# Performance work log

Measured on AMD Instinct MI355X. Metric: run time of the kernel, lower is better.

Reference implementation:

```python
import jax, jax.numpy as jnp
from jax import lax
import numpy as np

D_MODEL, D_STATE, D_CONV, EXPAND = 1024, 16, 4, 2
D_INNER = EXPAND * D_MODEL          # 2048
DT_RANK = D_MODEL // 16             # 64
B_SZ, L_SEQ = 2, 2048


def setup_inputs() -> dict:
    key = jax.random.key(0)
    ks = jax.random.split(key, 8)
    x = jax.random.normal(ks[0], (B_SZ, L_SEQ, D_MODEL), jnp.float32)
    inp = {
        "x": x,
        "ln_g": jnp.ones((D_MODEL,), jnp.float32),
        "ln_b": jnp.zeros((D_MODEL,), jnp.float32),
        # fan-in scaled weights for numerical sanity
        "W_in": jax.random.normal(ks[1], (2 * D_INNER, D_MODEL), jnp.float32) / np.sqrt(D_MODEL),
        "conv_w": jax.random.normal(ks[2], (D_INNER, D_CONV), jnp.float32) / np.sqrt(D_CONV),
        "conv_b": jnp.zeros((D_INNER,), jnp.float32),
        "W_xp": jax.random.normal(ks[3], (DT_RANK + 2 * D_STATE, D_INNER), jnp.float32) / np.sqrt(D_INNER),
        "W_dt": jax.random.normal(ks[4], (D_INNER, DT_RANK), jnp.float32) / np.sqrt(DT_RANK),
        "b_dt": jax.random.normal(ks[5], (D_INNER,), jnp.float32) * 0.1 - 4.0,  # softplus(dt) small, like mamba init
        # S4D-real init: A = -exp(A_log), A_log = log(1..d_state)
        "A_log": jnp.broadcast_to(jnp.log(jnp.arange(1, D_STATE + 1, dtype=jnp.float32)), (D_INNER, D_STATE)).copy(),
        "D": jnp.ones((D_INNER,), jnp.float32),
        "W_out": jax.random.normal(ks[6], (D_MODEL, D_INNER), jnp.float32) / np.sqrt(D_INNER),
    }
    return inp


def _selective_scan(u, dt, A, Bm, Cm, Dvec):
    # u, dt: (B, L, d_inner); Bm, Cm: (B, L, d_state); A: (d_inner, d_state)
    def step(h, inputs):
        u_t, dt_t, B_t, C_t = inputs                      # (B,di),(B,di),(B,n),(B,n)
        dA = jnp.exp(dt_t[:, :, None] * A[None])          # (B,di,n), in (0,1) since A<0
        dBu = (dt_t * u_t)[:, :, None] * B_t[:, None, :]  # (B,di,n)
        h = dA * h + dBu
        y = jnp.einsum('bdn,bn->bd', h, C_t)
        return h, y
    xs = (u.transpose(1, 0, 2), dt.transpose(1, 0, 2),
          Bm.transpose(1, 0, 2), Cm.transpose(1, 0, 2))
    h0 = jnp.zeros((u.shape[0], u.shape[2], A.shape[1]), u.dtype)
    _, ys = lax.scan(step, h0, xs)
    return ys.transpose(1, 0, 2) + u * Dvec               # (B, L, d_inner)


def reference(x, ln_g, ln_b, W_in, conv_w, conv_b, W_xp, W_dt, b_dt, A_log, D, W_out):
    d_inner, d_conv = conv_w.shape
    dt_rank = W_dt.shape[1]
    d_state = A_log.shape[1]
    # pre-LayerNorm
    mu = jnp.mean(x, axis=-1, keepdims=True)
    var = jnp.mean(jnp.square(x - mu), axis=-1, keepdims=True)
    xn = (x - mu) * lax.rsqrt(var + 1e-5) * ln_g + ln_b
    # input projection -> (B, L, 2*d_inner)
    xz = jnp.einsum('bld,ed->ble', xn, W_in)
    u, z = jnp.split(xz, 2, axis=-1)
    # causal depthwise conv over time
    u_c = lax.conv_general_dilated(
        u.transpose(0, 2, 1),                 # (B, d_inner, L)
        conv_w[:, None, :],                   # (d_inner, 1, d_conv)
        window_strides=(1,), padding=[(d_conv - 1, 0)],
        feature_group_count=d_inner)
    u_c = jax.nn.silu((u_c + conv_b[None, :, None]).transpose(0, 2, 1))  # (B, L, d_inner)
    # data-dependent dt, B, C
    x_dbl = jnp.einsum('bld,ed->ble', u_c, W_xp)
    dt, Bm, Cm = jnp.split(x_dbl, [dt_rank, dt_rank + d_state], axis=-1)
    dt = jax.nn.softplus(jnp.einsum('blr,dr->bld', dt, W_dt) + b_dt)
    A = -jnp.exp(A_log)
    y = _selective_scan(u_c, dt, A, Bm, Cm, D)
    y = y * jax.nn.silu(z)
    out = jnp.einsum('ble,de->bld', y, W_out)
    return x + out
```

## Files before the change

### kernel.cpp

```cpp
#include <hip/hip_runtime.h>

typedef __bf16 bf16x8 __attribute__((ext_vector_type(8)));
typedef float  f32x4  __attribute__((ext_vector_type(4)));

#define LOG2E 1.44269504088896f

__device__ __forceinline__ float bfl(unsigned short s) {
    return __uint_as_float(((unsigned int)s) << 16);
}
__device__ __forceinline__ unsigned short f2bf(float f) {
    unsigned int x = __float_as_uint(f);
    x += 0x7fffu + ((x >> 16) & 1u);
    return (unsigned short)(x >> 16);
}
__device__ __forceinline__ float fexp2(float x) { return __builtin_amdgcn_exp2f(x); }
__device__ __forceinline__ float fexp(float x)  { return __builtin_amdgcn_exp2f(x * LOG2E); }
__device__ __forceinline__ float frcp(float x)  { return __builtin_amdgcn_rcpf(x); }
__device__ __forceinline__ float silu_f(float x) {
    return x * frcp(1.f + fexp2(-x * LOG2E));
}
__device__ __forceinline__ void gl_lds(const unsigned short* g, unsigned short* l) {
    __builtin_amdgcn_global_load_lds(
        (__attribute__((address_space(1))) const void*)g,
        (__attribute__((address_space(3))) void*)l, 16, 0, 0);
}

#define BSZ   2
#define LSEQ  2048
#define DMODEL 1024
#define DI    2048
#define DS    16
#define NCH   64
#define CL    32

#define WI_N   4194304
#define WXP_N  196608
#define WDT_N  131072
#define WOUT_N 2097152
#define WSEG1  (WI_N)
#define WSEG2  (WI_N + WXP_N)
#define WSEG3  (WI_N + WXP_N + WDT_N)
#define WTOT   (WI_N + WXP_N + WDT_N + WOUT_N)

__global__ __launch_bounds__(256) void cvt_weights(
    const float* __restrict__ w0, const float* __restrict__ w1,
    const float* __restrict__ w2, const float* __restrict__ w3,
    unsigned short* __restrict__ dst)
{
    const size_t e0 = ((size_t)blockIdx.x * 256 + threadIdx.x) * 8;
    if (e0 >= WTOT) return;
    const float* src;
    size_t off;
    if      (e0 < WSEG1) { src = w0; off = e0; }
    else if (e0 < WSEG2) { src = w1; off = e0 - WSEG1; }
    else if (e0 < WSEG3) { src = w2; off = e0 - WSEG2; }
    else                 { src = w3; off = e0 - WSEG3; }
    float4 a = *(const float4*)(src + off);
    float4 b = *(const float4*)(src + off + 4);
    ushort4 lo, hi;
    lo.x = f2bf(a.x); lo.y = f2bf(a.y); lo.z = f2bf(a.z); lo.w = f2bf(a.w);
    hi.x = f2bf(b.x); hi.y = f2bf(b.y); hi.z = f2bf(b.z); hi.w = f2bf(b.w);
    *(ushort4*)(dst + e0) = lo;
    *(ushort4*)(dst + e0 + 4) = hi;
}

__global__ __launch_bounds__(256) void ln_kernel(
    const float* __restrict__ x,
    const float* __restrict__ g,
    const float* __restrict__ b,
    unsigned short* __restrict__ xn)
{
    const int row = blockIdx.x;
    const int tid = threadIdx.x;
    const int lane = tid & 63, wv = tid >> 6;
    const float* xp = x + (size_t)row * DMODEL;

    float4 v = ((const float4*)xp)[tid];
    float s = v.x + v.y + v.z + v.w;
    float q = v.x*v.x + v.y*v.y + v.z*v.z + v.w*v.w;
    #pragma unroll
    for (int o = 32; o > 0; o >>= 1) {
        s += __shfl_down(s, o);
        q += __shfl_down(q, o);
    }
    __shared__ float ss[4], sq[4];
    if (lane == 0) { ss[wv] = s; sq[wv] = q; }
    __syncthreads();
    s = ss[0] + ss[1] + ss[2] + ss[3];
    q = sq[0] + sq[1] + sq[2] + sq[3];
    const float mu  = s * (1.f / DMODEL);
    const float var = q * (1.f / DMODEL) - mu * mu;
    const float rs  = rsqrtf(var + 1e-5f);

    float4 gv = ((const float4*)g)[tid];
    float4 bv = ((const float4*)b)[tid];
    ushort4 o;
    o.x = f2bf((v.x - mu) * rs * gv.x + bv.x);
    o.y = f2bf((v.y - mu) * rs * gv.y + bv.y);
    o.z = f2bf((v.z - mu) * rs * gv.z + bv.z);
    o.w = f2bf((v.w - mu) * rs * gv.w + bv.w);
    ((ushort4*)(xn + (size_t)row * DMODEL))[tid] = o;
}

template<int EPI, int LOGM>
__global__ __launch_bounds__(512, 2) void gemm_pipe256(
    const unsigned short* __restrict__ A,
    const unsigned short* __restrict__ Bw,
    void* __restrict__ Cout,
    const void* __restrict__ aux0,
    int K, int ldc)
{
    __shared__ unsigned short As[2][256 * 64];
    __shared__ unsigned short Bs[2][256 * 64];
    const int tid  = threadIdx.x;
    const int lane = tid & 63;
    const int wid  = tid >> 6;
    const int wm   = (wid >> 2) * 128;
    const int wn   = (wid & 3) * 64;

    const int nwg = gridDim.x;
    const int id  = blockIdx.x;
    const int swz = (id & 7) * (nwg >> 3) + (id >> 3);
    const int bx  = swz & ((1 << LOGM) - 1);
    const int by  = swz >> LOGM;
    const size_t am0 = (size_t)bx * 256;
    const size_t bn0 = (size_t)by * 256;

    const int srow  = lane >> 3;
    const int sslot = (lane & 7) ^ srow;
    const unsigned short* gA = A  + (am0 + wid * 8 + srow) * (size_t)K + sslot * 8;
    const unsigned short* gB = Bw + (bn0 + wid * 8 + srow) * (size_t)K + sslot * 8;

    const int NT = K >> 6;

#define STAGE256(buf, ko)                                                      \
    {   _Pragma("unroll")                                                      \
        for (int j = 0; j < 4; ++j)                                            \
            gl_lds(gA + (size_t)(j * 64) * K + (ko), &As[buf][(j * 64 + wid * 8) * 64]); \
        _Pragma("unroll")                                                      \
        for (int j = 0; j < 4; ++j)                                            \
            gl_lds(gB + (size_t)(j * 64) * K + (ko), &Bs[buf][(j * 64 + wid * 8) * 64]); }

    STAGE256(0, 0)
    STAGE256(1, 64)

    f32x4 acc[8][4];
    f32x4 z4 = {0.f, 0.f, 0.f, 0.f};
    #pragma unroll
    for (int i = 0; i < 8; ++i)
        #pragma unroll
        for (int j = 0; j < 4; ++j) acc[i][j] = z4;

    const int lr  = lane & 15;
    const int lq  = lane >> 4;
    const int key = lr & 7;

#define RD_A(dst, q)                                                           \
    _Pragma("unroll")                                                          \
    for (int i = 0; i < 2; ++i)                                                \
        _Pragma("unroll")                                                      \
        for (int ks = 0; ks < 2; ++ks)                                         \
            dst[i][ks] = *(const bf16x8*)&As[cur][(wm + ((q) * 2 + i) * 16 + lr) * 64 \
                                                  + (((ks * 4 + lq) ^ key) * 8)];

#define MFMA_Q(src, q)                                                         \
    _Pragma("unroll")                                                          \
    for (int i = 0; i < 2; ++i)                                                \
        _Pragma("unroll")                                                      \
        for (int fn = 0; fn < 4; ++fn) {                                       \
            acc[(q) * 2 + i][fn] = __builtin_amdgcn_mfma_f32_16x16x32_bf16(    \
                src[i][0], bfv[fn][0], acc[(q) * 2 + i][fn], 0, 0, 0);         \
            acc[(q) * 2 + i][fn] = __builtin_amdgcn_mfma_f32_16x16x32_bf16(    \
                src[i][1], bfv[fn][1], acc[(q) * 2 + i][fn], 0, 0, 0);         }

    for (int t = 0; t < NT; ++t) {
        const int cur = t & 1;
        if (t < NT - 1) asm volatile("s_waitcnt vmcnt(8)" ::: "memory");
        else            asm volatile("s_waitcnt vmcnt(0)" ::: "memory");
        __builtin_amdgcn_s_barrier();
        __builtin_amdgcn_sched_barrier(0);

        bf16x8 bfv[4][2], fA[2][2], fB[2][2];
        #pragma unroll
        for (int fn = 0; fn < 4; ++fn)
            #pragma unroll
            for (int ks = 0; ks < 2; ++ks)
                bfv[fn][ks] = *(const bf16x8*)&Bs[cur][(wn + fn * 16 + lr) * 64
                                                        + (((ks * 4 + lq) ^ key) * 8)];
        RD_A(fA, 0)
        asm volatile("s_waitcnt lgkmcnt(0)" ::: "memory");
        __builtin_amdgcn_sched_barrier(0);

        RD_A(fB, 1)
        __builtin_amdgcn_s_setprio(1);
        MFMA_Q(fA, 0)
        __builtin_amdgcn_s_setprio(0);
        asm volatile("s_waitcnt lgkmcnt(0)" ::: "memory");
        __builtin_amdgcn_sched_barrier(0);

        RD_A(fA, 2)
        __builtin_amdgcn_s_setprio(1);
        MFMA_Q(fB, 1)
        __builtin_amdgcn_s_setprio(0);
        asm volatile("s_waitcnt lgkmcnt(0)" ::: "memory");
        __builtin_amdgcn_sched_barrier(0);

        RD_A(fB, 3)
        __builtin_amdgcn_s_setprio(1);
        MFMA_Q(fA, 2)
        __builtin_amdgcn_s_setprio(0);
        asm volatile("s_waitcnt lgkmcnt(0)" ::: "memory");
        __builtin_amdgcn_sched_barrier(0);

        __builtin_amdgcn_s_barrier();
        if (t + 2 < NT) {
            STAGE256(cur, (size_t)(t + 2) * 64)
        }
        __builtin_amdgcn_s_setprio(1);
        MFMA_Q(fB, 3)
        __builtin_amdgcn_s_setprio(0);
    }
#undef RD_A
#undef MFMA_Q
#undef STAGE256

    asm volatile("s_waitcnt vmcnt(0) lgkmcnt(0)" ::: "memory");
    __builtin_amdgcn_s_barrier();

    const int er = lq * 4;
    const int ec = lr;
    if constexpr (EPI == 0) {
        unsigned short* cw = &As[0][0] + wid * (16 * 88);
        const int rl  = lane >> 2;
        const int c8l = lane & 3;
        unsigned short* cbase = (unsigned short*)Cout;
        #pragma unroll
        for (int fm = 0; fm < 8; ++fm) {
            #pragma unroll
            for (int fn = 0; fn < 4; ++fn)
                #pragma unroll
                for (int r = 0; r < 4; ++r)
                    cw[(er + r) * 88 + fn * 16 + ec] = f2bf(acc[fm][fn][r]);
            #pragma unroll
            for (int u = 0; u < 2; ++u) {
                const int c8 = c8l + 4 * u;
                bf16x8 v = *(const bf16x8*)&cw[rl * 88 + c8 * 8];
                const size_t row = am0 + wm + fm * 16 + rl;
                const size_t col = bn0 + wn + c8 * 8;
                *(bf16x8*)(cbase + row * (size_t)ldc + col) = v;
            }
        }
    } else {
        #pragma unroll
        for (int fm = 0; fm < 8; ++fm) {
            #pragma unroll
            for (int fn = 0; fn < 4; ++fn) {
                const size_t col = bn0 + wn + fn * 16 + ec;
                #pragma unroll
                for (int r = 0; r < 4; ++r) {
                    const size_t row = am0 + wm + fm * 16 + er + r;
                    float t2 = acc[fm][fn][r] + ((const float*)aux0)[row * ldc + col];
                    ((float*)Cout)[row * ldc + col] = t2;
                }
            }
        }
    }
}

template<int EPI, int LOGNB>
__global__ __launch_bounds__(512, 2) void gemm_pipe128(
    const unsigned short* __restrict__ A,
    const unsigned short* __restrict__ Bw,
    void* __restrict__ Cout,
    const void* __restrict__ aux0,
    int K, int ldc)
{
    __shared__ unsigned short As[2][128 * 64];
    __shared__ unsigned short Bs[2][128 * 64];
    const int tid  = threadIdx.x;
    const int lane = tid & 63;
    const int wid  = tid >> 6;
    const int wm   = (wid >> 2) * 64;
    const int wn   = (wid & 3) * 32;

    const int nwg = gridDim.x;
    const int id  = blockIdx.x;
    const int swz = (id & 7) * (nwg >> 3) + (id >> 3);
    const int bn_i = swz & ((1 << LOGNB) - 1);
    const int bm_i = swz >> LOGNB;
    const size_t am0 = (size_t)bm_i * 128;
    const size_t bn0 = (size_t)bn_i * 128;

    const int srow  = lane >> 3;
    const int sslot = (lane & 7) ^ srow;
    const unsigned short* gA = A  + (am0 + wid * 16 + srow) * (size_t)K + sslot * 8;
    const unsigned short* gB = Bw + (bn0 + wid * 16 + srow) * (size_t)K + sslot * 8;

    const int NT = K >> 6;

#define STAGE128(buf, ko)                                                      \
    {   _Pragma("unroll")                                                      \
        for (int j = 0; j < 2; ++j)                                            \
            gl_lds(gA + (size_t)(j * 8) * K + (ko), &As[buf][(wid * 16 + j * 8) * 64]); \
        _Pragma("unroll")                                                      \
        for (int j = 0; j < 2; ++j)                                            \
            gl_lds(gB + (size_t)(j * 8) * K + (ko), &Bs[buf][(wid * 16 + j * 8) * 64]); }

    STAGE128(0, 0)
    STAGE128(1, 64)

    f32x4 acc[4][2];
    f32x4 z4 = {0.f, 0.f, 0.f, 0.f};
    #pragma unroll
    for (int i = 0; i < 4; ++i) { acc[i][0] = z4; acc[i][1] = z4; }

    const int lr  = lane & 15;
    const int lq  = lane >> 4;
    const int key = lr & 7;

#define RD_A128(dst, h)                                                        \
    _Pragma("unroll")                                                          \
    for (int i = 0; i < 2; ++i)                                                \
        _Pragma("unroll")                                                      \
        for (int ks = 0; ks < 2; ++ks)                                         \
            dst[i][ks] = *(const bf16x8*)&As[cur][(wm + ((h) * 2 + i) * 16 + lr) * 64 \
                                                  + (((ks * 4 + lq) ^ key) * 8)];

#define MFMA_H(src, h)                                                         \
    _Pragma("unroll")                                                          \
    for (int i = 0; i < 2; ++i)                                                \
        _Pragma("unroll")                                                      \
        for (int fn = 0; fn < 2; ++fn) {                                       \
            acc[(h) * 2 + i][fn] = __builtin_amdgcn_mfma_f32_16x16x32_bf16(    \
                src[i][0], bfv[fn][0], acc[(h) * 2 + i][fn], 0, 0, 0);         \
            acc[(h) * 2 + i][fn] = __builtin_amdgcn_mfma_f32_16x16x32_bf16(    \
                src[i][1], bfv[fn][1], acc[(h) * 2 + i][fn], 0, 0, 0);         }

    for (int t = 0; t < NT; ++t) {
        const int cur = t & 1;
        if (t < NT - 1) asm volatile("s_waitcnt vmcnt(4)" ::: "memory");
        else            asm volatile("s_waitcnt vmcnt(0)" ::: "memory");
        __builtin_amdgcn_s_barrier();
        __builtin_amdgcn_sched_barrier(0);

        bf16x8 bfv[2][2], fA[2][2], fB[2][2];
        #pragma unroll
        for (int fn = 0; fn < 2; ++fn)
            #pragma unroll
            for (int ks = 0; ks < 2; ++ks)
                bfv[fn][ks] = *(const bf16x8*)&Bs[cur][(wn + fn * 16 + lr) * 64
                                                        + (((ks * 4 + lq) ^ key) * 8)];
        RD_A128(fA, 0)
        asm volatile("s_waitcnt lgkmcnt(0)" ::: "memory");
        __builtin_amdgcn_sched_barrier(0);

        RD_A128(fB, 1)
        __builtin_amdgcn_s_setprio(1);
        MFMA_H(fA, 0)
        __builtin_amdgcn_s_setprio(0);
        asm volatile("s_waitcnt lgkmcnt(0)" ::: "memory");
        __builtin_amdgcn_sched_barrier(0);

        __builtin_amdgcn_s_barrier();
        if (t + 2 < NT) {
            STAGE128(cur, (size_t)(t + 2) * 64)
        }
        __builtin_amdgcn_s_setprio(1);
        MFMA_H(fB, 1)
        __builtin_amdgcn_s_setprio(0);
    }
#undef RD_A128
#undef MFMA_H
#undef STAGE128

    const int er = lq * 4;
    const int ec = lr;
    #pragma unroll
    for (int fm = 0; fm < 4; ++fm) {
        #pragma unroll
        for (int fn = 0; fn < 2; ++fn) {
            const size_t col = bn0 + wn + fn * 16 + ec;
            #pragma unroll
            for (int r = 0; r < 4; ++r) {
                const size_t row = am0 + wm + fm * 16 + er + r;
                float v = acc[fm][fn][r];
                if constexpr (EPI == 0) {
                    ((unsigned short*)Cout)[row * ldc + col] = f2bf(v);
                } else {
                    float t2 = v + ((const float*)aux0)[row * ldc + col];
                    ((float*)Cout)[row * ldc + col] = t2;
                }
            }
        }
    }
}

template<int BM, int BN, int EPI, int LOG_NBXM>
__global__ __launch_bounds__(256) void gemm_lds(
    const unsigned short* __restrict__ A,
    const unsigned short* __restrict__ Bw,
    void* __restrict__ Cout,
    const void* __restrict__ aux0,
    int K, int ldc)
{
    constexpr int FM = BM / 32;
    constexpr int FN = BN / 32;
    __shared__ unsigned short As[BM * 64];
    __shared__ unsigned short Bs[BN * 64];
    const int tid  = threadIdx.x;
    const int lane = tid & 63;
    const int wv   = tid >> 6;
    const int wm   = (wv >> 1) * (BM / 2);
    const int wn   = (wv & 1)  * (BN / 2);

    const int nwg = gridDim.x;
    const int id  = blockIdx.x;
    const int swz = (id & 7) * (nwg >> 3) + (id >> 3);
    const int bx  = swz & ((1 << LOG_NBXM) - 1);
    const int by  = swz >> LOG_NBXM;

    f32x4 acc[FM][FN];
    f32x4 z4 = {0.f, 0.f, 0.f, 0.f};
    #pragma unroll
    for (int i = 0; i < FM; ++i)
        #pragma unroll
        for (int j = 0; j < FN; ++j) acc[i][j] = z4;

    const size_t am0 = (size_t)bx * BM;
    const size_t bn0 = (size_t)by * BN;
    const int srow  = lane >> 3;
    const int scol  = (lane & 7) * 8;

    for (int k0 = 0; k0 < K; k0 += 64) {
        __syncthreads();
        #pragma unroll
        for (int i = 0; i < BM / 32; ++i) {
            const int rb = (wv * (BM / 32) + i) * 8;
            gl_lds(&A[(am0 + rb + srow) * (size_t)K + k0 + scol], &As[rb * 64]);
        }
        #pragma unroll
        for (int i = 0; i < BN / 32; ++i) {
            const int rb = (wv * (BN / 32) + i) * 8;
            gl_lds(&Bw[(bn0 + rb + srow) * (size_t)K + k0 + scol], &Bs[rb * 64]);
        }
        __syncthreads();
        const int lr = lane & 15, lk = (lane >> 4) * 8;
        #pragma unroll
        for (int ks = 0; ks < 2; ++ks) {
            bf16x8 af[FM], bfv[FN];
            #pragma unroll
            for (int fm = 0; fm < FM; ++fm)
                af[fm] = *(const bf16x8*)&As[(wm + fm * 16 + lr) * 64 + ks * 32 + lk];
            #pragma unroll
            for (int fn = 0; fn < FN; ++fn)
                bfv[fn] = *(const bf16x8*)&Bs[(wn + fn * 16 + lr) * 64 + ks * 32 + lk];
            #pragma unroll
            for (int fm = 0; fm < FM; ++fm)
                #pragma unroll
                for (int fn = 0; fn < FN; ++fn)
                    acc[fm][fn] = __builtin_amdgcn_mfma_f32_16x16x32_bf16(
                        af[fm], bfv[fn], acc[fm][fn], 0, 0, 0);
        }
    }

    const int er = (lane >> 4) * 4;
    const int ec = lane & 15;
    #pragma unroll
    for (int fm = 0; fm < FM; ++fm) {
        #pragma unroll
        for (int fn = 0; fn < FN; ++fn) {
            const size_t col = bn0 + wn + fn * 16 + ec;
            #pragma unroll
            for (int r = 0; r < 4; ++r) {
                const size_t row = am0 + wm + fm * 16 + er + r;
                float v = acc[fm][fn][r];
                if constexpr (EPI == 0) {
                    ((unsigned short*)Cout)[row * ldc + col] = f2bf(v);
                } else if constexpr (EPI == 2) {
                    float t = v + ((const float*)aux0)[col];
                    float e = fexp2(t * LOG2E);
                    float sp = 0.69314718056f * __builtin_amdgcn_logf(1.f + e);
                    if (t > 20.f) sp = t;
                    ((unsigned short*)Cout)[row * ldc + col] = f2bf(sp);
                } else {
                    float t = v + ((const float*)aux0)[row * ldc + col];
                    ((float*)Cout)[row * ldc + col] = t;
                }
            }
        }
    }
}

__global__ __launch_bounds__(256) void gemm4_splitk(
    const unsigned short* __restrict__ A,
    const unsigned short* __restrict__ Bw,
    float* __restrict__ Cpart)
{
    constexpr int LDP = 72;
    __shared__ unsigned short As[64 * LDP];
    __shared__ unsigned short Bs[96 * LDP];
    const int tid  = threadIdx.x;
    const int lane = tid & 63;
    const int wv   = tid >> 6;
    const int wm   = (wv >> 1) * 32;
    const int wn   = (wv & 1)  * 48;

    f32x4 acc[2][3];
    f32x4 z4 = {0.f, 0.f, 0.f, 0.f};
    #pragma unroll
    for (int i = 0; i < 2; ++i)
        #pragma unroll
        for (int j = 0; j < 3; ++j) acc[i][j] = z4;

    const size_t am0 = (size_t)blockIdx.x * 64;
    const int kz = blockIdx.y;
    const int kbeg = kz * 256;
    const int r0 = tid >> 3;
    const int c0 = (tid & 7) * 8;

    for (int k0 = kbeg; k0 < kbeg + 256; k0 += 64) {
        __syncthreads();
        #pragma unroll
        for (int p = 0; p < 2; ++p) {
            int r = r0 + p * 32;
            *(uint4*)&As[r * LDP + c0] = *(const uint4*)&A[(am0 + r) * (size_t)2048 + k0 + c0];
        }
        #pragma unroll
        for (int p = 0; p < 3; ++p) {
            int r = r0 + p * 32;
            *(uint4*)&Bs[r * LDP + c0] = *(const uint4*)&Bw[(size_t)r * 2048 + k0 + c0];
        }
        __syncthreads();
        const int lr = lane & 15, lk = (lane >> 4) * 8;
        #pragma unroll
        for (int ks = 0; ks < 2; ++ks) {
            bf16x8 af[2], bfv[3];
            #pragma unroll
            for (int fm = 0; fm < 2; ++fm)
                af[fm] = *(const bf16x8*)&As[(wm + fm * 16 + lr) * LDP + ks * 32 + lk];
            #pragma unroll
            for (int fn = 0; fn < 3; ++fn)
                bfv[fn] = *(const bf16x8*)&Bs[(wn + fn * 16 + lr) * LDP + ks * 32 + lk];
            #pragma unroll
            for (int fm = 0; fm < 2; ++fm)
                #pragma unroll
                for (int fn = 0; fn < 3; ++fn)
                    acc[fm][fn] = __builtin_amdgcn_mfma_f32_16x16x32_bf16(
                        af[fm], bfv[fn], acc[fm][fn], 0, 0, 0);
        }
    }

    const int er = (lane >> 4) * 4;
    const int ec = lane & 15;
    float* out = Cpart + (size_t)kz * 4096 * 96;
    #pragma unroll
    for (int fm = 0; fm < 2; ++fm) {
        #pragma unroll
        for (int fn = 0; fn < 3; ++fn) {
            const int col = wn + fn * 16 + ec;
            #pragma unroll
            for (int r = 0; r < 4; ++r) {
                const size_t row = am0 + wm + fm * 16 + er + r;
                out[row * 96 + col] = acc[fm][fn][r];
            }
        }
    }
}

__global__ __launch_bounds__(256) void reduce_xdbl(
    const float* __restrict__ Cpart,
    float* __restrict__ x_dbl,
    unsigned short* __restrict__ dtlow)
{
    const int e = blockIdx.x * 256 + threadIdx.x;
    float s = 0.f;
    #pragma unroll
    for (int kz = 0; kz < 8; ++kz) s += Cpart[(size_t)kz * 393216 + e];
    x_dbl[e] = s;
    const int row = e / 96, col = e - row * 96;
    if (col < 64) dtlow[row * 64 + col] = f2bf(s);
}

__global__ __launch_bounds__(256) void conv_silu(
    const unsigned short* __restrict__ xz,
    const float* __restrict__ convw,
    const float* __restrict__ convb,
    unsigned short* __restrict__ u_c)
{
    const size_t i = (size_t)blockIdx.x * 256 + threadIdx.x;
    if (i >= (size_t)BSZ * LSEQ * DI) return;
    const int d = (int)(i & (DI - 1));
    const size_t bl = i >> 11;
    const int l = (int)(bl & (LSEQ - 1));
    const int b = (int)(bl >> 11);

    float4 wv = *(const float4*)&convw[d * 4];
    float acc = convb[d];
    const size_t rowbase = (size_t)(b * LSEQ) * (2 * DI) + d;
    if (l >= 3) acc += bfl(xz[rowbase + (size_t)(l - 3) * (2 * DI)]) * wv.x;
    if (l >= 2) acc += bfl(xz[rowbase + (size_t)(l - 2) * (2 * DI)]) * wv.y;
    if (l >= 1) acc += bfl(xz[rowbase + (size_t)(l - 1) * (2 * DI)]) * wv.z;
    acc += bfl(xz[rowbase + (size_t)l * (2 * DI)]) * wv.w;
    u_c[i] = f2bf(silu_f(acc));
}

__device__ __forceinline__ bool load_A(const float* __restrict__ A_log, int d, float* An2) {
    bool fast = true;
    #pragma unroll
    for (int i = 0; i < 4; ++i) {
        float4 a = *(const float4*)&A_log[(size_t)d * DS + i * 4];
        float e0 = fexp(a.x), e1 = fexp(a.y), e2 = fexp(a.z), e3 = fexp(a.w);
        fast = fast && fabsf(e0 - (4*i+1)) < 1e-3f * (4*i+1)
                    && fabsf(e1 - (4*i+2)) < 1e-3f * (4*i+2)
                    && fabsf(e2 - (4*i+3)) < 1e-3f * (4*i+3)
                    && fabsf(e3 - (4*i+4)) < 1e-3f * (4*i+4);
        An2[4*i+0] = -e0 * LOG2E; An2[4*i+1] = -e1 * LOG2E;
        An2[4*i+2] = -e2 * LOG2E; An2[4*i+3] = -e3 * LOG2E;
    }
    return fast;
}

__global__ __launch_bounds__(256) void scan1(
    const unsigned short* __restrict__ dt,
    const unsigned short* __restrict__ u_c,
    const float* __restrict__ x_dbl,
    const float* __restrict__ A_log,
    float* __restrict__ chunk_h,
    float* __restrict__ Ssum)
{
    const int d = blockIdx.x * 256 + threadIdx.x;
    const int b = blockIdx.y, c = blockIdx.z;
    const int tid = threadIdx.x;

    __shared__ float sB[CL][DS];
    if (tid < 128) {
        int s = tid >> 2, j = (tid & 3) * 4;
        *(float4*)&sB[s][j] =
            *(const float4*)&x_dbl[(size_t)(b * LSEQ + c * CL + s) * 96 + 64 + j];
    }

    float An2[DS];
    const bool fast = load_A(A_log, d, An2);
    __syncthreads();

    float h[DS];
    #pragma unroll
    for (int n = 0; n < DS; ++n) h[n] = 0.f;
    float S = 0.f;
    const size_t base = (size_t)(b * LSEQ + c * CL) * DI + d;
    if (fast) {
        for (int s = 0; s < CL; ++s) {
            float dtt = bfl(dt[base + (size_t)s * DI]);
            float ut  = bfl(u_c[base + (size_t)s * DI]);
            S += dtt;
            float dtu = dtt * ut;
            float e1 = fexp2(-dtt * LOG2E);
            float p = 1.f;
            #pragma unroll
            for (int n = 0; n < DS; ++n) {
                p *= e1;
                h[n] = p * h[n] + dtu * sB[s][n];
            }
        }
    } else {
        for (int s = 0; s < CL; ++s) {
            float dtt = bfl(dt[base + (size_t)s * DI]);
            float ut  = bfl(u_c[base + (size_t)s * DI]);
            S += dtt;
            float dtu = dtt * ut;
            #pragma unroll
            for (int n = 0; n < DS; ++n) {
                float dA = fexp2(dtt * An2[n]);
                h[n] = dA * h[n] + dtu * sB[s][n];
            }
        }
    }
    const size_t co = ((size_t)((b * NCH + c) * DI) + d) * DS;
    #pragma unroll
    for (int n = 0; n < DS; ++n) chunk_h[co + n] = h[n];
    Ssum[(size_t)(b * NCH + c) * DI + d] = S;
}

__global__ __launch_bounds__(256) void scan2(
    float* __restrict__ chunk_h,
    const float* __restrict__ Ssum,
    const float* __restrict__ A_log)
{
    const int gid = blockIdx.x * 256 + threadIdx.x;
    const int b = gid >> 15;
    const int rem = gid & 32767;
    const int d = rem >> 4;
    const int n = rem & 15;
    const float A2 = -fexp(A_log[(size_t)d * DS + n]) * LOG2E;
    float H = 0.f;
    for (int c = 0; c < NCH; ++c) {
        const size_t idx = ((size_t)((b * NCH + c) * DI) + d) * DS + n;
        float hl = chunk_h[idx];
        float S  = Ssum[(size_t)(b * NCH + c) * DI + d];
        chunk_h[idx] = H;
        H = fexp2(A2 * S) * H + hl;
    }
}

__global__ __launch_bounds__(256) void scan3(
    const unsigned short* __restrict__ dt,
    const unsigned short* __restrict__ u_c,
    const float* __restrict__ x_dbl,
    const float* __restrict__ A_log,
    const float* __restrict__ Hstart,
    const float* __restrict__ Dvec,
    const unsigned short* __restrict__ xz,
    unsigned short* __restrict__ yb)
{
    const int d = blockIdx.x * 256 + threadIdx.x;
    const int b = blockIdx.y, c = blockIdx.z;
    const int tid = threadIdx.x;

    __shared__ float sBC[CL][32];
    {
        int s = tid >> 3, j = (tid & 7) * 4;
        *(float4*)&sBC[s][j] =
            *(const float4*)&x_dbl[(size_t)(b * LSEQ + c * CL + s) * 96 + 64 + j];
    }

    float An2[DS];
    const bool fast = load_A(A_log, d, An2);
    const float Dd = Dvec[d];
    float h[DS];
    const size_t co = ((size_t)((b * NCH + c) * DI) + d) * DS;
    #pragma unroll
    for (int n = 0; n < DS; ++n) h[n] = Hstart[co + n];
    __syncthreads();

    const size_t base  = (size_t)(b * LSEQ + c * CL) * DI + d;
    const size_t zbase = (size_t)(b * LSEQ + c * CL) * (2 * DI) + DI + d;
    if (fast) {
        for (int s = 0; s < CL; ++s) {
            float dtt = bfl(dt[base + (size_t)s * DI]);
            float ut  = bfl(u_c[base + (size_t)s * DI]);
            float dtu = dtt * ut;
            float e1 = fexp2(-dtt * LOG2E);
            float p = 1.f;
            float a0 = 0.f, a1 = 0.f;
            #pragma unroll
            for (int n = 0; n < DS; ++n) {
                p *= e1;
                h[n] = p * h[n] + dtu * sBC[s][n];
                if (n & 1) a1 += h[n] * sBC[s][16 + n];
                else       a0 += h[n] * sBC[s][16 + n];
            }
            float y = a0 + a1 + Dd * ut;
            float z = bfl(xz[zbase + (size_t)s * (2 * DI)]);
            yb[base + (size_t)s * DI] = f2bf(y * silu_f(z));
        }
    } else {
        for (int s = 0; s < CL; ++s) {
            float dtt = bfl(dt[base + (size_t)s * DI]);
            float ut  = bfl(u_c[base + (size_t)s * DI]);
            float dtu = dtt * ut;
            float a0 = 0.f, a1 = 0.f;
            #pragma unroll
            for (int n = 0; n < DS; ++n) {
                float dA = fexp2(dtt * An2[n]);
                h[n] = dA * h[n] + dtu * sBC[s][n];
                if (n & 1) a1 += h[n] * sBC[s][16 + n];
                else       a0 += h[n] * sBC[s][16 + n];
            }
            float y = a0 + a1 + Dd * ut;
            float z = bfl(xz[zbase + (size_t)s * (2 * DI)]);
            yb[base + (size_t)s * DI] = f2bf(y * silu_f(z));
        }
    }
}

extern "C" void kernel_launch(void* const* d_in, const int* in_sizes, int n_in,
                              void* d_out, int out_size, void* d_ws, size_t ws_size,
                              hipStream_t stream) {
    const float* x      = (const float*)d_in[0];
    const float* ln_g   = (const float*)d_in[1];
    const float* ln_b   = (const float*)d_in[2];
    const float* W_in   = (const float*)d_in[3];
    const float* conv_w = (const float*)d_in[4];
    const float* conv_b = (const float*)d_in[5];
    const float* W_xp   = (const float*)d_in[6];
    const float* W_dt   = (const float*)d_in[7];
    const float* b_dt   = (const float*)d_in[8];
    const float* A_log  = (const float*)d_in[9];
    const float* Dv     = (const float*)d_in[10];
    const float* W_out  = (const float*)d_in[11];
    float* out = (float*)d_out;

    char* w = (char*)d_ws;
    unsigned short* xn     = (unsigned short*)(w + 0);
    unsigned short* xz     = (unsigned short*)(w + 8388608);
    unsigned short* u_c    = (unsigned short*)(w + 41943040);
    float*          x_dbl  = (float*)         (w + 58720256);
    unsigned short* dtlow  = (unsigned short*)(w + 60293120);
    unsigned short* dtb    = (unsigned short*)(w + 60817408);
    float*          chunkh = (float*)         (w + 77594624);
    float*          Ssum   = (float*)         (w + 94371840);
    unsigned short* yb     = (unsigned short*)(w + 95420416);
    unsigned short* wbf    = (unsigned short*)(w + 112197632);
    float*          Cpart  = (float*)         (w + 125435904);
    unsigned short* Wi_bf   = wbf;
    unsigned short* Wxp_bf  = wbf + WSEG1;
    unsigned short* Wdt_bf  = wbf + WSEG2;
    unsigned short* Wout_bf = wbf + WSEG3;
    (void)in_sizes; (void)n_in; (void)out_size; (void)ws_size;

    const int MROWS = BSZ * LSEQ;

    cvt_weights<<<(WTOT / 8 + 255) / 256, 256, 0, stream>>>(
        W_in, W_xp, W_dt, W_out, wbf);
    ln_kernel<<<MROWS, 256, 0, stream>>>(x, ln_g, ln_b, xn);
    gemm_pipe256<0, 4><<<256, 512, 0, stream>>>(
        xn, Wi_bf, xz, nullptr, DMODEL, 2 * DI);
    conv_silu<<<(MROWS * DI) / 256, 256, 0, stream>>>(xz, conv_w, conv_b, u_c);
    gemm4_splitk<<<dim3(64, 8), 256, 0, stream>>>(u_c, Wxp_bf, Cpart);
    reduce_xdbl<<<(MROWS * 96) / 256, 256, 0, stream>>>(Cpart, x_dbl, dtlow);
    gemm_lds<128, 64, 2, 5><<<1024, 256, 0, stream>>>(
        dtlow, Wdt_bf, dtb, b_dt, 64, DI);
    scan1<<<dim3(DI / 256, BSZ, NCH), 256, 0, stream>>>(
        dtb, u_c, x_dbl, A_log, chunkh, Ssum);
    scan2<<<(BSZ * DI * DS) / 256, 256, 0, stream>>>(chunkh, Ssum, A_log);
    scan3<<<dim3(DI / 256, BSZ, NCH), 256, 0, stream>>>(
        dtb, u_c, x_dbl, A_log, chunkh, Dv, xz, yb);
    gemm_pipe128<3, 3><<<256, 512, 0, stream>>>(
        yb, Wout_bf, out, x, DI, DMODEL);
}
```

Measured before the change: 180.0 us.

## Merge layernorm with weight conversion, fold z-silu into GEMM epilogue, lengthen scan chunks

Merges the weight-conversion and layernorm kernels into one launch by splitting blocks between the two jobs. Applies silu to the z half of the input projection inside the GEMM epilogue, so the scan's final pass only multiplies by the stored value. Doubles the scan chunk length (32 to 64) and halves the chunk count, adjusting the shared-memory B/C loads to match. Fewer chunks mean less chunk-carry work but less parallelism in scan1 and scan3, and the z tensor is now stored after silu in bf16.

After: 188.5 us. +4.7%, slower.

```diff
diff --git a/kernel.cpp b/kernel.cpp
--- a/kernel.cpp
+++ b/kernel.cpp
@@ -30,8 +30,8 @@
 #define DMODEL 1024
 #define DI    2048
 #define DS    16
-#define NCH   64
-#define CL    32
+#define NCH   32
+#define CL    64
 
 #define WI_N   4194304
 #define WXP_N  196608
@@ -41,65 +41,65 @@
 #define WSEG2  (WI_N + WXP_N)
 #define WSEG3  (WI_N + WXP_N + WDT_N)
 #define WTOT   (WI_N + WXP_N + WDT_N + WOUT_N)
-
-__global__ __launch_bounds__(256) void cvt_weights(
+#define CVT_BLOCKS 3232
+
+__global__ __launch_bounds__(256) void ln_cvt(
+    const float* __restrict__ x,
+    const float* __restrict__ g,
+    const float* __restrict__ b,
+    unsigned short* __restrict__ xn,
     const float* __restrict__ w0, const float* __restrict__ w1,
     const float* __restrict__ w2, const float* __restrict__ w3,
     unsigned short* __restrict__ dst)
 {
-    const size_t e0 = ((size_t)blockIdx.x * 256 + threadIdx.x) * 8;
-    if (e0 >= WTOT) return;
-    const float* src;
-    size_t off;
-    if      (e0 < WSEG1) { src = w0; off = e0; }
-    else if (e0 < WSEG2) { src = w1; off = e0 - WSEG1; }
-    else if (e0 < WSEG3) { src = w2; off = e0 - WSEG2; }
-    else                 { src = w3; off = e0 - WSEG3; }
-    float4 a = *(const float4*)(src + off);
-    float4 b = *(const float4*)(src + off + 4);
-    ushort4 lo, hi;
-    lo.x = f2bf(a.x); lo.y = f2bf(a.y); lo.z = f2bf(a.z); lo.w = f2bf(a.w);
-    hi.x = f2bf(b.x); hi.y = f2bf(b.y); hi.z = f2bf(b.z); hi.w = f2bf(b.w);
-    *(ushort4*)(dst + e0) = lo;
-    *(ushort4*)(dst + e0 + 4) = hi;
-}
-
-__global__ __launch_bounds__(256) void ln_kernel(
-    const float* __restrict__ x,
-    const float* __restrict__ g,
-    const float* __restrict__ b,
-    unsigned short* __restrict__ xn)
-{
-    const int row = blockIdx.x;
     const int tid = threadIdx.x;
-    const int lane = tid & 63, wv = tid >> 6;
-    const float* xp = x + (size_t)row * DMODEL;
-
-    float4 v = ((const float4*)xp)[tid];
-    float s = v.x + v.y + v.z + v.w;
-    float q = v.x*v.x + v.y*v.y + v.z*v.z + v.w*v.w;
-    #pragma unroll
-    for (int o = 32; o > 0; o >>= 1) {
-        s += __shfl_down(s, o);
-        q += __shfl_down(q, o);
-    }
-    __shared__ float ss[4], sq[4];
-    if (lane == 0) { ss[wv] = s; sq[wv] = q; }
-    __syncthreads();
-    s = ss[0] + ss[1] + ss[2] + ss[3];
-    q = sq[0] + sq[1] + sq[2] + sq[3];
-    const float mu  = s * (1.f / DMODEL);
-    const float var = q * (1.f / DMODEL) - mu * mu;
-    const float rs  = rsqrtf(var + 1e-5f);
-
-    float4 gv = ((const float4*)g)[tid];
-    float4 bv = ((const float4*)b)[tid];
-    ushort4 o;
-    o.x = f2bf((v.x - mu) * rs * gv.x + bv.x);
-    o.y = f2bf((v.y - mu) * rs * gv.y + bv.y);
-    o.z = f2bf((v.z - mu) * rs * gv.z + bv.z);
-    o.w = f2bf((v.w - mu) * rs * gv.w + bv.w);
-    ((ushort4*)(xn + (size_t)row * DMODEL))[tid] = o;
+    if (blockIdx.x < BSZ * LSEQ) {
+        const int row = blockIdx.x;
+        const int lane = tid & 63, wv = tid >> 6;
+        const float* xp = x + (size_t)row * DMODEL;
+
+        float4 v = ((const float4*)xp)[tid];
+        float s = v.x + v.y + v.z + v.w;
+        float q = v.x*v.x + v.y*v.y + v.z*v.z + v.w*v.w;
+        #pragma unroll
+        for (int o = 32; o > 0; o >>= 1) {
+            s += __shfl_down(s, o);
+            q += __shfl_down(q, o);
+        }
+        __shared__ float ss[4], sq[4];
+        if (lane == 0) { ss[wv] = s; sq[wv] = q; }
+        __syncthreads();
+        s = ss[0] + ss[1] + ss[2] + ss[3];
+        q = sq[0] + sq[1] + sq[2] + sq[3];
+        const float mu  = s * (1.f / DMODEL);
+        const float var = q * (1.f / DMODEL) - mu * mu;
+        const float rs  = rsqrtf(var + 1e-5f);
+
+        float4 gv = ((const float4*)g)[tid];
+        float4 bv = ((const float4*)b)[tid];
+        ushort4 o;
+        o.x = f2bf((v.x - mu) * rs * gv.x + bv.x);
+        o.y = f2bf((v.y - mu) * rs * gv.y + bv.y);
+        o.z = f2bf((v.z - mu) * rs * gv.z + bv.z);
+        o.w = f2bf((v.w - mu) * rs * gv.w + bv.w);
+        ((ushort4*)(xn + (size_t)row * DMODEL))[tid] = o;
+    } else {
+        const size_t e0 = ((size_t)(blockIdx.x - BSZ * LSEQ) * 256 + tid) * 8;
+        if (e0 >= WTOT) return;
+        const float* src;
+        size_t off;
+        if      (e0 < WSEG1) { src = w0; off = e0; }
+        else if (e0 < WSEG2) { src = w1; off = e0 - WSEG1; }
+        else if (e0 < WSEG3) { src = w2; off = e0 - WSEG2; }
+        else                 { src = w3; off = e0 - WSEG3; }
+        float4 a = *(const float4*)(src + off);
+        float4 bb = *(const float4*)(src + off + 4);
+        ushort4 lo, hi;
+        lo.x = f2bf(a.x);  lo.y = f2bf(a.y);  lo.z = f2bf(a.z);  lo.w = f2bf(a.w);
+        hi.x = f2bf(bb.x); hi.y = f2bf(bb.y); hi.z = f2bf(bb.z); hi.w = f2bf(bb.w);
+        *(ushort4*)(dst + e0) = lo;
+        *(ushort4*)(dst + e0 + 4) = hi;
+    }
 }
 
 template<int EPI, int LOGM>
@@ -230,6 +230,7 @@
     const int er = lq * 4;
     const int ec = lr;
     if constexpr (EPI == 0) {
+        const bool zhalf = (bn0 >= (size_t)DI);
         unsigned short* cw = &As[0][0] + wid * (16 * 88);
         const int rl  = lane >> 2;
         const int c8l = lane & 3;
@@ -239,8 +240,11 @@
             #pragma unroll
             for (int fn = 0; fn < 4; ++fn)
                 #pragma unroll
-                for (int r = 0; r < 4; ++r)
-                    cw[(er + r) * 88 + fn * 16 + ec] = f2bf(acc[fm][fn][r]);
+                for (int r = 0; r < 4; ++r) {
+                    float v = acc[fm][fn][r];
+                    if (zhalf) v = silu_f(v);
+                    cw[(er + r) * 88 + fn * 16 + ec] = f2bf(v);
+                }
             #pragma unroll
             for (int u = 0; u < 2; ++u) {
                 const int c8 = c8l + 4 * u;
@@ -633,7 +637,7 @@
     const int tid = threadIdx.x;
 
     __shared__ float sB[CL][DS];
-    if (tid < 128) {
+    {
         int s = tid >> 2, j = (tid & 3) * 4;
         *(float4*)&sB[s][j] =
             *(const float4*)&x_dbl[(size_t)(b * LSEQ + c * CL + s) * 96 + 64 + j];
@@ -718,9 +722,11 @@
 
     __shared__ float sBC[CL][32];
     {
-        int s = tid >> 3, j = (tid & 7) * 4;
+        int s = tid >> 2, j = (tid & 3) * 8;
         *(float4*)&sBC[s][j] =
             *(const float4*)&x_dbl[(size_t)(b * LSEQ + c * CL + s) * 96 + 64 + j];
+        *(float4*)&sBC[s][j + 4] =
+            *(const float4*)&x_dbl[(size_t)(b * LSEQ + c * CL + s) * 96 + 64 + j + 4];
     }
 
     float An2[DS];
@@ -750,8 +756,8 @@
                 else       a0 += h[n] * sBC[s][16 + n];
             }
             float y = a0 + a1 + Dd * ut;
-            float z = bfl(xz[zbase + (size_t)s * (2 * DI)]);
-            yb[base + (size_t)s * DI] = f2bf(y * silu_f(z));
+            float zs = bfl(xz[zbase + (size_t)s * (2 * DI)]);
+            yb[base + (size_t)s * DI] = f2bf(y * zs);
         }
     } else {
         for (int s = 0; s < CL; ++s) {
@@ -767,8 +773,8 @@
                 else       a0 += h[n] * sBC[s][16 + n];
             }
             float y = a0 + a1 + Dd * ut;
-            float z = bfl(xz[zbase + (size_t)s * (2 * DI)]);
-            yb[base + (size_t)s * DI] = f2bf(y * silu_f(z));
+            float zs = bfl(xz[zbase + (size_t)s * (2 * DI)]);
+            yb[base + (size_t)s * DI] = f2bf(y * zs);
         }
     }
 }
@@ -810,9 +816,8 @@
 
     const int MROWS = BSZ * LSEQ;
 
-    cvt_weights<<<(WTOT / 8 + 255) / 256, 256, 0, stream>>>(
-        W_in, W_xp, W_dt, W_out, wbf);
-    ln_kernel<<<MROWS, 256, 0, stream>>>(x, ln_g, ln_b, xn);
+    ln_cvt<<<MROWS + CVT_BLOCKS, 256, 0, stream>>>(
+        x, ln_g, ln_b, xn, W_in, W_xp, W_dt, W_out, wbf);
     gemm_pipe256<0, 4><<<256, 512, 0, stream>>>(
         xn, Wi_bf, xz, nullptr, DMODEL, 2 * DI);
     conv_silu<<<(MROWS * DI) / 256, 256, 0, stream>>>(xz, conv_w, conv_b, u_c);
```
